# Optimization experiments

Hardware: AMD Instinct MI355X
Metric: run time of the kernel (lower is better)

The kernel has to match this reference:

```python
import jax, jax.numpy as jnp
import numpy as np

EMBED = 1024
HEADS = 16
HEAD_DIM = EMBED // HEADS


def setup_inputs() -> dict:
    key = jax.random.key(0)
    ks = jax.random.split(key, 8)
    N, S = 4, 2048
    inp = {
        "values": jax.random.normal(ks[0], (N, S, EMBED), dtype=jnp.float32),
        "keys": jax.random.normal(ks[1], (N, S, EMBED), dtype=jnp.float32),
        "queries": jax.random.normal(ks[2], (N, S, EMBED), dtype=jnp.float32),
        # Linear weights stored as [in, out] (torch Linear applies x @ W.T; here W already transposed)
        "W_v": jax.random.normal(ks[3], (EMBED, EMBED), dtype=jnp.float32) / np.sqrt(EMBED),
        "W_k": jax.random.normal(ks[4], (EMBED, EMBED), dtype=jnp.float32) / np.sqrt(EMBED),
        "W_q": jax.random.normal(ks[5], (EMBED, EMBED), dtype=jnp.float32) / np.sqrt(EMBED),
        "W_o": jax.random.normal(ks[6], (EMBED, EMBED), dtype=jnp.float32) / np.sqrt(EMBED),
        "b_o": jax.random.normal(ks[7], (EMBED,), dtype=jnp.float32) * 0.01,
    }
    return inp


def reference(values, keys, queries, W_v, W_k, W_q, W_o, b_o):
    N, q_len, _ = queries.shape
    v = (values @ W_v).reshape(N, -1, HEADS, HEAD_DIM)   # [n, v_len, h, d]
    k = (keys @ W_k).reshape(N, -1, HEADS, HEAD_DIM)     # [n, k_len, h, d]
    q = (queries @ W_q).reshape(N, -1, HEADS, HEAD_DIM)  # [n, q_len, h, d]
    # NOTE: original scales by sqrt(embed_size), not sqrt(head_dim)
    energy = jnp.einsum('nqhd,nkhd->nhqk', q, k) / jnp.sqrt(jnp.float32(EMBED))
    attn = jax.nn.softmax(energy, axis=-1)
    out = jnp.einsum('nhqk,nkhd->nqhd', attn, v).reshape(N, q_len, EMBED)
    return out @ W_o + b_o
```

## Files before the change

kernel.cpp:

```cpp
#include <hip/hip_runtime.h>
#include <hip/hip_bf16.h>
#include <stdint.h>

typedef __attribute__((ext_vector_type(8))) short short8;
typedef __attribute__((ext_vector_type(4))) float f32x4;
typedef __attribute__((ext_vector_type(4))) unsigned short u16x4;
typedef unsigned short u16;

#define EMBED 1024
#define SEQ 2048
#define NBATCH 4
#define MROWS (NBATCH * SEQ)

__device__ __forceinline__ u16 f2bf(float f) {
  union { float f; uint32_t u; } v; v.f = f;
  uint32_t r = v.u + 0x7fffu + ((v.u >> 16) & 1u);
  return (u16)(r >> 16);
}

__device__ __forceinline__ uint32_t cvtpk(float lo, float hi) {
  uint32_t r;
  asm("v_cvt_pk_bf16_f32 %0, %1, %2" : "=v"(r) : "v"(lo), "v"(hi));
  return r;
}

__device__ __forceinline__ float exp2a(float x) {
#if __has_builtin(__builtin_amdgcn_exp2f)
  return __builtin_amdgcn_exp2f(x);
#else
  return exp2f(x);
#endif
}

__device__ __forceinline__ void gld16(const void* g, void* l) {
  __builtin_amdgcn_global_load_lds((const __attribute__((address_space(1))) void*)g,
                                   (__attribute__((address_space(3))) void*)l, 16, 0, 0);
}

__global__ __launch_bounds__(256) void cvt_bf16_kernel(const float4* __restrict__ in,
                                                       u16x4* __restrict__ out, int n4) {
  int stride = gridDim.x * blockDim.x;
  for (int i = blockIdx.x * blockDim.x + threadIdx.x; i < n4; i += stride) {
    float4 v = in[i];
    u16x4 o = { f2bf(v.x), f2bf(v.y), f2bf(v.z), f2bf(v.w) };
    out[i] = o;
  }
}

__global__ __launch_bounds__(256) void wtrans_kernel(const float* __restrict__ W,
                                                     u16* __restrict__ Wt) {
  __shared__ float tile[32][33];
  int bx = blockIdx.x * 32, by = blockIdx.y * 32;
  int tx = threadIdx.x & 31, ty = threadIdx.x >> 5;
#pragma unroll
  for (int i = 0; i < 32; i += 8)
    tile[ty + i][tx] = W[(size_t)(by + ty + i) * EMBED + bx + tx];
  __syncthreads();
#pragma unroll
  for (int i = 0; i < 32; i += 8)
    Wt[(size_t)(bx + ty + i) * EMBED + by + tx] = f2bf(tile[tx][ty + i]);
}

template <int EPI>
__global__ __launch_bounds__(256) void gemm_bt(const u16* __restrict__ A,
                                               const u16* __restrict__ Bt,
                                               void* __restrict__ outp,
                                               const float* __restrict__ bias,
                                               float oscale) {
  constexpr int K = 1024;
  __shared__ u16 lsA[128 * 64];
  __shared__ u16 lsB[128 * 64];
  const int t = threadIdx.x, l = t & 63, w = t >> 6;
  const int g = l >> 4, r15 = l & 15;
  const int m0 = blockIdx.y * 128, n0 = blockIdx.x * 128;
  const int wm = (w >> 1) * 64, wn = (w & 1) * 64;
  f32x4 acc[4][4] = {};
  const int srow = t >> 3;
  const int sc16 = (t & 7) * 16;

  const u16* Ap[4]; const u16* Bp[4];
#pragma unroll
  for (int j = 0; j < 4; ++j) {
    int row = srow + j * 32;
    int colswz = (sc16 ^ ((row & 7) << 4)) >> 1;
    Ap[j] = A  + (size_t)(m0 + row) * K + colswz;
    Bp[j] = Bt + (size_t)(n0 + row) * K + colswz;
  }

  for (int k0 = 0; k0 < K; k0 += 64) {
#pragma unroll
    for (int j = 0; j < 4; ++j) {
      gld16(Ap[j] + k0, lsA + j * 2048 + w * 512);
      gld16(Bp[j] + k0, lsB + j * 2048 + w * 512);
    }
    __syncthreads();
    short8 af[2][4], bfv[2][4];
#pragma unroll
    for (int kk = 0; kk < 2; ++kk) {
#pragma unroll
      for (int mi = 0; mi < 4; ++mi) {
        int row = wm + mi * 16 + r15;
        af[kk][mi] = *(const short8*)((const char*)lsA + row * 128 + ((kk * 64 + g * 16) ^ ((row & 7) << 4)));
      }
#pragma unroll
      for (int ni = 0; ni < 4; ++ni) {
        int row = wn + ni * 16 + r15;
        bfv[kk][ni] = *(const short8*)((const char*)lsB + row * 128 + ((kk * 64 + g * 16) ^ ((row & 7) << 4)));
      }
    }
#pragma unroll
    for (int kk = 0; kk < 2; ++kk)
#pragma unroll
      for (int mi = 0; mi < 4; ++mi)
#pragma unroll
        for (int ni = 0; ni < 4; ++ni)
          acc[mi][ni] = __builtin_amdgcn_mfma_f32_16x16x32_bf16(af[kk][mi], bfv[kk][ni], acc[mi][ni], 0, 0, 0);
    __syncthreads();
  }

#pragma unroll
  for (int mi = 0; mi < 4; ++mi)
#pragma unroll
    for (int ni = 0; ni < 4; ++ni)
#pragma unroll
      for (int r = 0; r < 4; ++r) {
        int row = m0 + wm + mi * 16 + g * 4 + r;
        int col = n0 + wn + ni * 16 + r15;
        float v = acc[mi][ni][r];
        if (EPI == 0) {
          ((u16*)outp)[(((size_t)(row >> 11) * 16 + (col >> 6)) * SEQ + (row & 2047)) * 64 + (col & 63)] = f2bf(v * oscale);
        } else if (EPI == 1) {
          ((u16*)outp)[(((size_t)(row >> 11) * 16 + (col >> 6)) * 64 + (col & 63)) * SEQ + (row & 2047)] = f2bf(v);
        } else {
          ((float*)outp)[(size_t)row * EMBED + col] = v + bias[col];
        }
      }
}

__global__ __launch_bounds__(256) void attn_kernel(const u16* __restrict__ Q,
                                                   const u16* __restrict__ Kb,
                                                   const u16* __restrict__ Vt,
                                                   u16* __restrict__ AO) {
  __shared__ u16 lsK[2][64 * 64];
  __shared__ u16 lsV[2][64 * 64];
  const int t = threadIdx.x, l = t & 63, w = t >> 6;
  const int g = l >> 4, r15 = l & 15;

  const int flat = blockIdx.x;
  const int work = (flat & 7) * 128 + (flat >> 3);
  const int bh = work >> 4;
  const int q0 = (work & 15) * 128;

  const u16* Qh = Q + (size_t)bh * SEQ * 64;
  const u16* Kh = Kb + (size_t)bh * SEQ * 64;
  const u16* Vh = Vt + (size_t)bh * 64 * SEQ;

  short8 qf[2][2];
#pragma unroll
  for (int qi = 0; qi < 2; ++qi)
#pragma unroll
    for (int dh = 0; dh < 2; ++dh)
      qf[qi][dh] = *(const short8*)&Qh[(size_t)(q0 + w * 32 + qi * 16 + r15) * 64 + dh * 32 + g * 8];

  float mrun[2] = { -1e30f, -1e30f }, lsum[2] = { 0.f, 0.f };
  f32x4 oacc[4][2] = {};

  const int srow = t >> 3;
  const int scolb = (t & 7) * 16;

  uint4 vreg[2];

  auto STAGE_K = [&](int buf, int kv0) {
#pragma unroll
    for (int j = 0; j < 2; ++j) {
      int row = j * 32 + srow;
      int colswz = (scolb ^ ((row & 7) << 4)) >> 1;
      gld16(Kh + (size_t)(kv0 + row) * 64 + colswz, &lsK[buf][j * 2048 + w * 512]);
    }
  };
  auto VLOAD = [&](int kv0) {
#pragma unroll
    for (int j = 0; j < 2; ++j) {
      int row = j * 32 + srow;
      vreg[j] = *(const uint4*)(Vh + (size_t)row * SEQ + kv0 + (scolb >> 1));
    }
  };
  auto VSTORE = [&](int buf) {
#pragma unroll
    for (int j = 0; j < 2; ++j) {
      int row = j * 32 + srow;
      int c4 = (row & 7) << 4, c3 = ((row >> 3) & 1) << 3;
      char* base = (char*)&lsV[buf][0] + row * 128 + (scolb ^ c4);
      *(uint2*)(base + c3)       = make_uint2(vreg[j].x, vreg[j].y);
      *(uint2*)(base + (8 ^ c3)) = make_uint2(vreg[j].z, vreg[j].w);
    }
  };

  VLOAD(0);
  STAGE_K(0, 0);
  VSTORE(0);
  asm volatile("s_waitcnt vmcnt(0) lgkmcnt(0)" ::: "memory");
  __builtin_amdgcn_s_barrier();

  int cur = 0;
  for (int kv = 0; kv < SEQ / 64; ++kv) {
    const bool more = (kv + 1 < SEQ / 64);
    if (more) {
      VLOAD((kv + 1) * 64);
      STAGE_K(cur ^ 1, (kv + 1) * 64);
    }

    const u16* Kc = lsK[cur];
    const u16* Vc = lsV[cur];

    f32x4 sacc[2][4] = {};
    __builtin_amdgcn_s_setprio(1);
#pragma unroll
    for (int c = 0; c < 4; ++c) {
      int krow = c * 16 + r15;
      int sz = (krow & 7) << 4;
#pragma unroll
      for (int dh = 0; dh < 2; ++dh) {
        short8 kf = *(const short8*)((const char*)Kc + krow * 128 + ((dh * 64 + g * 16) ^ sz));
#pragma unroll
        for (int qi = 0; qi < 2; ++qi)
          sacc[qi][c] = __builtin_amdgcn_mfma_f32_16x16x32_bf16(kf, qf[qi][dh], sacc[qi][c], 0, 0, 0);
      }
    }
    __builtin_amdgcn_s_setprio(0);

    float mt[2];
#pragma unroll
    for (int qi = 0; qi < 2; ++qi) {
      const f32x4* s = sacc[qi];
      float t0 = fmaxf(fmaxf(s[0][0], s[0][1]), s[0][2]);
      float t1 = fmaxf(fmaxf(s[0][3], s[1][0]), s[1][1]);
      float t2 = fmaxf(fmaxf(s[1][2], s[1][3]), s[2][0]);
      float t3 = fmaxf(fmaxf(s[2][1], s[2][2]), s[2][3]);
      float t4 = fmaxf(fmaxf(s[3][0], s[3][1]), s[3][2]);
      float m = fmaxf(fmaxf(t0, t1), fmaxf(fmaxf(t2, t3), fmaxf(t4, s[3][3])));
      m = fmaxf(m, __shfl_xor(m, 16, 64));
      m = fmaxf(m, __shfl_xor(m, 32, 64));
      mt[qi] = m;
    }

    int ok = (mt[0] <= mrun[0] + 8.f) && (mt[1] <= mrun[1] + 8.f);
    if (!__all(ok)) {
#pragma unroll
      for (int qi = 0; qi < 2; ++qi) {
        float mn = fmaxf(mrun[qi], mt[qi]);
        float al = exp2a(mrun[qi] - mn);
        mrun[qi] = mn;
        lsum[qi] *= al;
#pragma unroll
        for (int dc = 0; dc < 4; ++dc)
#pragma unroll
          for (int r = 0; r < 4; ++r)
            oacc[dc][qi][r] *= al;
      }
    }

    short8 pb[2][2];
#pragma unroll
    for (int qi = 0; qi < 2; ++qi) {
      float s0 = 0.f;
#pragma unroll
      for (int c = 0; c < 4; ++c)
#pragma unroll
        for (int r = 0; r < 4; ++r) {
          float p = exp2a(sacc[qi][c][r] - mrun[qi]);
          sacc[qi][c][r] = p;
          s0 += p;
        }
      lsum[qi] += s0;
#pragma unroll
      for (int kh = 0; kh < 2; ++kh) {
        union { uint32_t u[4]; short8 s; } pu;
        pu.u[0] = cvtpk(sacc[qi][2 * kh][0],     sacc[qi][2 * kh][1]);
        pu.u[1] = cvtpk(sacc[qi][2 * kh][2],     sacc[qi][2 * kh][3]);
        pu.u[2] = cvtpk(sacc[qi][2 * kh + 1][0], sacc[qi][2 * kh + 1][1]);
        pu.u[3] = cvtpk(sacc[qi][2 * kh + 1][2], sacc[qi][2 * kh + 1][3]);
        pb[qi][kh] = pu.s;
      }
    }

    __builtin_amdgcn_s_setprio(1);
#pragma unroll
    for (int dc = 0; dc < 4; ++dc) {
      int vrow = dc * 16 + r15;
      int sz = ((vrow & 7) << 4) | (((vrow >> 3) & 1) << 3);
      const char* vb = (const char*)Vc + vrow * 128;
#pragma unroll
      for (int kh = 0; kh < 2; ++kh) {
        union { uint2 v[2]; short8 s; } va;
        va.v[0] = *(const uint2*)(vb + ((kh * 64 + 8 * g) ^ sz));
        va.v[1] = *(const uint2*)(vb + ((kh * 64 + 32 + 8 * g) ^ sz));
#pragma unroll
        for (int qi = 0; qi < 2; ++qi)
          oacc[dc][qi] = __builtin_amdgcn_mfma_f32_16x16x32_bf16(va.s, pb[qi][kh], oacc[dc][qi], 0, 0, 0);
      }
    }
    __builtin_amdgcn_s_setprio(0);

    if (more) VSTORE(cur ^ 1);
    asm volatile("s_waitcnt vmcnt(0) lgkmcnt(0)" ::: "memory");
    __builtin_amdgcn_s_barrier();
    cur ^= 1;
  }

  const int nb = bh >> 4, h = bh & 15;
#pragma unroll
  for (int qi = 0; qi < 2; ++qi) {
    float s = lsum[qi];
    s += __shfl_xor(s, 16, 64);
    s += __shfl_xor(s, 32, 64);
    lsum[qi] = 1.0f / s;
  }
#pragma unroll
  for (int dc = 0; dc < 4; ++dc)
#pragma unroll
    for (int qi = 0; qi < 2; ++qi) {
      int q = q0 + w * 32 + qi * 16 + r15;
      int d = dc * 16 + g * 4;
      uint32_t a = cvtpk(oacc[dc][qi][0] * lsum[qi], oacc[dc][qi][1] * lsum[qi]);
      uint32_t b = cvtpk(oacc[dc][qi][2] * lsum[qi], oacc[dc][qi][3] * lsum[qi]);
      uint2* dst = (uint2*)&AO[((size_t)(nb * SEQ + q)) * EMBED + h * 64 + d];
      *dst = make_uint2(a, b);
    }
}

extern "C" void kernel_launch(void* const* d_in, const int* in_sizes, int n_in,
                              void* d_out, int out_size, void* d_ws, size_t ws_size,
                              hipStream_t stream) {
  const float* values  = (const float*)d_in[0];
  const float* keys    = (const float*)d_in[1];
  const float* queries = (const float*)d_in[2];
  const float* W_v = (const float*)d_in[3];
  const float* W_k = (const float*)d_in[4];
  const float* W_q = (const float*)d_in[5];
  const float* W_o = (const float*)d_in[6];
  const float* b_o = (const float*)d_in[7];

  const size_t XSZ = (size_t)MROWS * EMBED;
  const size_t WSZ = (size_t)EMBED * EMBED;
  u16* ws = (u16*)d_ws;
  u16* Xv  = ws;
  u16* Xk  = ws + XSZ;
  u16* Xq  = ws + 2 * XSZ;
  u16* Wvt = ws + 3 * XSZ;
  u16* Wkt = Wvt + WSZ;
  u16* Wqt = Wkt + WSZ;
  u16* Wot = Wqt + WSZ;
  u16* Qb  = Wot + WSZ;
  u16* Kb  = Qb + XSZ;
  u16* Vtb = Kb + XSZ;
  u16* AO  = Xv;

  int n4 = (int)(XSZ / 4);
  cvt_bf16_kernel<<<1024, 256, 0, stream>>>((const float4*)values,  (u16x4*)Xv, n4);
  cvt_bf16_kernel<<<1024, 256, 0, stream>>>((const float4*)keys,    (u16x4*)Xk, n4);
  cvt_bf16_kernel<<<1024, 256, 0, stream>>>((const float4*)queries, (u16x4*)Xq, n4);

  dim3 tg(32, 32);
  wtrans_kernel<<<tg, 256, 0, stream>>>(W_v, Wvt);
  wtrans_kernel<<<tg, 256, 0, stream>>>(W_k, Wkt);
  wtrans_kernel<<<tg, 256, 0, stream>>>(W_q, Wqt);
  wtrans_kernel<<<tg, 256, 0, stream>>>(W_o, Wot);

  const float QSCALE = 0.03125f * 1.4426950408889634f;
  dim3 gg(EMBED / 128, MROWS / 128);
  gemm_bt<0><<<gg, 256, 0, stream>>>(Xq, Wqt, Qb, nullptr, QSCALE);
  gemm_bt<0><<<gg, 256, 0, stream>>>(Xk, Wkt, Kb, nullptr, 1.0f);
  gemm_bt<1><<<gg, 256, 0, stream>>>(Xv, Wvt, Vtb, nullptr, 1.0f);

  attn_kernel<<<1024, 256, 0, stream>>>(Qb, Kb, Vtb, AO);

  gemm_bt<2><<<gg, 256, 0, stream>>>(AO, Wot, d_out, b_o, 1.0f);
}
```

Before: 251.6 us.

## Batch prep launches, unroll attention loop by two, defer max shuffle

Merges the three bf16 conversion launches into one kernel and the four weight-transpose launches into one 3D-grid launch, cutting launch overhead. In the attention kernel, the KV loop is restructured into pairs of steps with fixed buffer indices. The cross-lane max shuffles now run only on the rare rescale path; the skip test uses per-lane maxima, with each lane's exponent still bounded by its own +8 check. The kernel also adds a 4-wave occupancy hint, uses an inline v_exp_f32, and swaps raw waitcnt+barrier for __syncthreads.

```diff
diff --git a/kernel.cpp b/kernel.cpp
--- a/kernel.cpp
+++ b/kernel.cpp
@@ -24,12 +24,10 @@
   return r;
 }
 
-__device__ __forceinline__ float exp2a(float x) {
-#if __has_builtin(__builtin_amdgcn_exp2f)
-  return __builtin_amdgcn_exp2f(x);
-#else
-  return exp2f(x);
-#endif
+__device__ __forceinline__ float vexp2(float x) {
+  float r;
+  asm("v_exp_f32 %0, %1" : "=v"(r) : "v"(x));
+  return r;
 }
 
 __device__ __forceinline__ void gld16(const void* g, void* l) {
@@ -37,18 +35,34 @@
                                    (__attribute__((address_space(3))) void*)l, 16, 0, 0);
 }
 
-__global__ __launch_bounds__(256) void cvt_bf16_kernel(const float4* __restrict__ in,
-                                                       u16x4* __restrict__ out, int n4) {
-  int stride = gridDim.x * blockDim.x;
-  for (int i = blockIdx.x * blockDim.x + threadIdx.x; i < n4; i += stride) {
+__global__ __launch_bounds__(256) void cvt3_kernel(const float4* __restrict__ a,
+                                                   const float4* __restrict__ b,
+                                                   const float4* __restrict__ c,
+                                                   u16x4* __restrict__ oa,
+                                                   u16x4* __restrict__ ob,
+                                                   u16x4* __restrict__ oc, int n4) {
+  int which = blockIdx.x >> 9;
+  const float4* in = which == 0 ? a : (which == 1 ? b : c);
+  u16x4* out = which == 0 ? oa : (which == 1 ? ob : oc);
+  int stride = 512 * 256;
+  for (int i = (blockIdx.x & 511) * 256 + threadIdx.x; i < n4; i += stride) {
     float4 v = in[i];
     u16x4 o = { f2bf(v.x), f2bf(v.y), f2bf(v.z), f2bf(v.w) };
     out[i] = o;
   }
 }
 
-__global__ __launch_bounds__(256) void wtrans_kernel(const float* __restrict__ W,
-                                                     u16* __restrict__ Wt) {
+__global__ __launch_bounds__(256) void wtrans_kernel(const float* __restrict__ W0,
+                                                     const float* __restrict__ W1,
+                                                     const float* __restrict__ W2,
+                                                     const float* __restrict__ W3,
+                                                     u16* __restrict__ T0,
+                                                     u16* __restrict__ T1,
+                                                     u16* __restrict__ T2,
+                                                     u16* __restrict__ T3) {
+  int z = blockIdx.z;
+  const float* W = z == 0 ? W0 : (z == 1 ? W1 : (z == 2 ? W2 : W3));
+  u16* Wt = z == 0 ? T0 : (z == 1 ? T1 : (z == 2 ? T2 : T3));
   __shared__ float tile[32][33];
   int bx = blockIdx.x * 32, by = blockIdx.y * 32;
   int tx = threadIdx.x & 31, ty = threadIdx.x >> 5;
@@ -137,10 +151,10 @@
       }
 }
 
-__global__ __launch_bounds__(256) void attn_kernel(const u16* __restrict__ Q,
-                                                   const u16* __restrict__ Kb,
-                                                   const u16* __restrict__ Vt,
-                                                   u16* __restrict__ AO) {
+__global__ __launch_bounds__(256, 4) void attn_kernel(const u16* __restrict__ Q,
+                                                      const u16* __restrict__ Kb,
+                                                      const u16* __restrict__ Vt,
+                                                      u16* __restrict__ AO) {
   __shared__ u16 lsK[2][64 * 64];
   __shared__ u16 lsV[2][64 * 64];
   const int t = threadIdx.x, l = t & 63, w = t >> 6;
@@ -196,22 +210,13 @@
     }
   };
 
-  VLOAD(0);
-  STAGE_K(0, 0);
-  VSTORE(0);
-  asm volatile("s_waitcnt vmcnt(0) lgkmcnt(0)" ::: "memory");
-  __builtin_amdgcn_s_barrier();
-
-  int cur = 0;
-  for (int kv = 0; kv < SEQ / 64; ++kv) {
-    const bool more = (kv + 1 < SEQ / 64);
-    if (more) {
-      VLOAD((kv + 1) * 64);
-      STAGE_K(cur ^ 1, (kv + 1) * 64);
-    }
-
-    const u16* Kc = lsK[cur];
-    const u16* Vc = lsV[cur];
+  auto STEP = [&](int buf, bool pre, int a) {
+    if (pre) {
+      VLOAD((a + 1) * 64);
+      STAGE_K(buf ^ 1, (a + 1) * 64);
+    }
+    const u16* Kc = lsK[buf];
+    const u16* Vc = lsV[buf];
 
     f32x4 sacc[2][4] = {};
     __builtin_amdgcn_s_setprio(1);
@@ -229,27 +234,28 @@
     }
     __builtin_amdgcn_s_setprio(0);
 
-    float mt[2];
+    float lmax[2];
 #pragma unroll
     for (int qi = 0; qi < 2; ++qi) {
       const f32x4* s = sacc[qi];
-      float t0 = fmaxf(fmaxf(s[0][0], s[0][1]), s[0][2]);
-      float t1 = fmaxf(fmaxf(s[0][3], s[1][0]), s[1][1]);
-      float t2 = fmaxf(fmaxf(s[1][2], s[1][3]), s[2][0]);
-      float t3 = fmaxf(fmaxf(s[2][1], s[2][2]), s[2][3]);
-      float t4 = fmaxf(fmaxf(s[3][0], s[3][1]), s[3][2]);
-      float m = fmaxf(fmaxf(t0, t1), fmaxf(fmaxf(t2, t3), fmaxf(t4, s[3][3])));
-      m = fmaxf(m, __shfl_xor(m, 16, 64));
-      m = fmaxf(m, __shfl_xor(m, 32, 64));
-      mt[qi] = m;
-    }
-
-    int ok = (mt[0] <= mrun[0] + 8.f) && (mt[1] <= mrun[1] + 8.f);
+      float m = s[0][0];
+#pragma unroll
+      for (int c = 0; c < 4; ++c)
+#pragma unroll
+        for (int r = 0; r < 4; ++r)
+          m = fmaxf(m, s[c][r]);
+      lmax[qi] = m;
+    }
+
+    int ok = (lmax[0] <= mrun[0] + 8.f) && (lmax[1] <= mrun[1] + 8.f);
     if (!__all(ok)) {
 #pragma unroll
       for (int qi = 0; qi < 2; ++qi) {
-        float mn = fmaxf(mrun[qi], mt[qi]);
-        float al = exp2a(mrun[qi] - mn);
+        float mt = lmax[qi];
+        mt = fmaxf(mt, __shfl_xor(mt, 16, 64));
+        mt = fmaxf(mt, __shfl_xor(mt, 32, 64));
+        float mn = fmaxf(mrun[qi], mt);
+        float al = vexp2(mrun[qi] - mn);
         mrun[qi] = mn;
         lsum[qi] *= al;
 #pragma unroll
@@ -268,7 +274,7 @@
       for (int c = 0; c < 4; ++c)
 #pragma unroll
         for (int r = 0; r < 4; ++r) {
-          float p = exp2a(sacc[qi][c][r] - mrun[qi]);
+          float p = vexp2(sacc[qi][c][r] - mrun[qi]);
           sacc[qi][c][r] = p;
           s0 += p;
         }
@@ -302,10 +308,19 @@
     }
     __builtin_amdgcn_s_setprio(0);
 
-    if (more) VSTORE(cur ^ 1);
-    asm volatile("s_waitcnt vmcnt(0) lgkmcnt(0)" ::: "memory");
-    __builtin_amdgcn_s_barrier();
-    cur ^= 1;
+    if (pre) VSTORE(buf ^ 1);
+    __syncthreads();
+  };
+
+  VLOAD(0);
+  STAGE_K(0, 0);
+  VSTORE(0);
+  __syncthreads();
+
+#pragma unroll 1
+  for (int pair = 0; pair < 16; ++pair) {
+    STEP(0, true, 2 * pair);
+    STEP(1, pair != 15, 2 * pair + 1);
   }
 
   const int nb = bh >> 4, h = bh & 15;
@@ -357,15 +372,11 @@
   u16* AO  = Xv;
 
   int n4 = (int)(XSZ / 4);
-  cvt_bf16_kernel<<<1024, 256, 0, stream>>>((const float4*)values,  (u16x4*)Xv, n4);
-  cvt_bf16_kernel<<<1024, 256, 0, stream>>>((const float4*)keys,    (u16x4*)Xk, n4);
-  cvt_bf16_kernel<<<1024, 256, 0, stream>>>((const float4*)queries, (u16x4*)Xq, n4);
-
-  dim3 tg(32, 32);
-  wtrans_kernel<<<tg, 256, 0, stream>>>(W_v, Wvt);
-  wtrans_kernel<<<tg, 256, 0, stream>>>(W_k, Wkt);
-  wtrans_kernel<<<tg, 256, 0, stream>>>(W_q, Wqt);
-  wtrans_kernel<<<tg, 256, 0, stream>>>(W_o, Wot);
+  cvt3_kernel<<<1536, 256, 0, stream>>>((const float4*)values, (const float4*)keys,
+                                        (const float4*)queries,
+                                        (u16x4*)Xv, (u16x4*)Xk, (u16x4*)Xq, n4);
+
+  wtrans_kernel<<<dim3(32, 32, 4), 256, 0, stream>>>(W_v, W_k, W_q, W_o, Wvt, Wkt, Wqt, Wot);
 
   const float QSCALE = 0.03125f * 1.4426950408889634f;
   dim3 gg(EMBED / 128, MROWS / 128);
```

Result: slower. 284.7 us (+13.1%).
